# Kernel tuning notes

Hardware: AMD Instinct MI355X
Metric: run time of the kernel (lower is better)

Reference implementation:

```python
import jax, jax.numpy as jnp
import numpy as np

# Model dims (ViT-Base @ 384)
L, H, D, HD, M, P, IMG, B, NC, CH = 12, 12, 768, 64, 3072, 16, 384, 32, 1000, 3
NPATCH = (IMG // P) ** 2  # 576
SCALE = 1.0 / np.sqrt(HD)


def setup_inputs() -> dict:
    key = jax.random.key(0)
    ks = iter(jax.random.split(key, 16))
    def n(shape, s=0.02):
        return (jax.random.normal(next(ks), shape, jnp.float32) * s).astype(jnp.float32)
    return dict(
        x=jax.random.normal(next(ks), (B, CH, IMG, IMG), jnp.float32),
        conv_w=n((D, CH, P, P)), conv_b=jnp.zeros((D,), jnp.float32),
        cls_token=jnp.zeros((1, 1, D), jnp.float32),
        pos_emb=n((1, NPATCH + 1, D), 1.0),
        ln1_g=jnp.ones((L, D), jnp.float32), ln1_b=jnp.zeros((L, D), jnp.float32),
        wqkv=n((L, H, D, 3 * HD)), bqkv=jnp.zeros((L, H, 3 * HD), jnp.float32),
        wmsa=n((L, D, D)), bmsa=jnp.zeros((L, D), jnp.float32),
        ln2_g=jnp.ones((L, D), jnp.float32), ln2_b=jnp.zeros((L, D), jnp.float32),
        lnm_g=jnp.ones((L, D), jnp.float32), lnm_b=jnp.zeros((L, D), jnp.float32),
        w1=n((L, D, M)), b1=jnp.zeros((L, M), jnp.float32),
        w2=n((L, M, D)), b2=jnp.zeros((L, D), jnp.float32),
        lnf_g=jnp.ones((D,), jnp.float32), lnf_b=jnp.zeros((D,), jnp.float32),
        whead=n((D, NC)), bhead=jnp.zeros((NC,), jnp.float32),
    )


def _ln(x, g, b, eps=1e-5):
    mu = jnp.mean(x, axis=-1, keepdims=True)
    var = jnp.mean(jnp.square(x - mu), axis=-1, keepdims=True)
    return (x - mu) * jax.lax.rsqrt(var + eps) * g + b


def _encoder_block(x, p):
    (ln1_g, ln1_b, wqkv, bqkv, wmsa, bmsa,
     ln2_g, ln2_b, lnm_g, lnm_b, w1, b1, w2, b2) = p
    b = x.shape[0]
    h = _ln(x, ln1_g, ln1_b)
    # batched per-head QKV (math identical to looping over H small Linears)
    qkv = jnp.einsum('bsd,hde->bhse', h, wqkv) + bqkv[:, None, :]  # [B,H,S,3*HD]
    q, k, v = jnp.split(qkv, 3, axis=-1)
    attn = jax.nn.softmax(jnp.einsum('bhqe,bhke->bhqk', q, k) * SCALE, axis=-1)
    o = jnp.einsum('bhqk,bhke->bhqe', attn, v)          # [B,H,S,HD]
    o = o.transpose(0, 2, 1, 3).reshape(b, -1, D)        # concat heads along feature
    msa = jnp.einsum('bsd,de->bse', o, wmsa) + bmsa
    x1 = h + msa                                          # residual around MSA (post-LN1)
    h2 = _ln(x1, ln2_g, ln2_b)
    h2 = _ln(h2, lnm_g, lnm_b)                            # MLPBlock's own LayerNorm (double LN, faithful)
    mlp = jnp.einsum('bsm,md->bsd', jax.nn.gelu(jnp.einsum('bsd,dm->bsm', h2, w1) + b1, approximate=False), w2) + b2
    return x1 + mlp, None


def reference(x, conv_w, conv_b, cls_token, pos_emb,
              ln1_g, ln1_b, wqkv, bqkv, wmsa, bmsa,
              ln2_g, ln2_b, lnm_g, lnm_b, w1, b1, w2, b2,
              lnf_g, lnf_b, whead, bhead):
    b = x.shape[0]
    # patchify conv (image divisible by patch, so F.pad is a no-op)
    t = jax.lax.conv_general_dilated(x, conv_w, (P, P), 'VALID',
                                     dimension_numbers=('NCHW', 'OIHW', 'NCHW'))
    t = t + conv_b[None, :, None, None]
    # faithful to torch .view(b, -1, embed_dim) on NCHW layout (channel-major flatten)
    t = t.reshape(b, -1, D)
    n = t.shape[1]
    t = jnp.concatenate([jnp.broadcast_to(cls_token, (b, 1, D)), t], axis=1)
    t = t + pos_emb[:, :n + 1]
    stacked = (ln1_g, ln1_b, wqkv, bqkv, wmsa, bmsa,
               ln2_g, ln2_b, lnm_g, lnm_b, w1, b1, w2, b2)
    t, _ = jax.lax.scan(_encoder_block, t, stacked)
    y = _ln(t[:, 0], lnf_g, lnf_b)
    y = jax.nn.softmax(jnp.einsum('bd,dc->bc', y, whead) + bhead, axis=-1)
    return y
```

## Files before the change

kernel.cpp:

```cpp
#include <hip/hip_runtime.h>

using f16   = _Float16;
using f16x8 = __attribute__((ext_vector_type(8))) _Float16;
using f32x4 = __attribute__((ext_vector_type(4))) float;

#define MPAD  18560
#define MREAL 18464
#define MCONV 18432
#define SEQ   577
#define SPAD  640
#define NHEAD 12
#define NBATCH 32
#define SCALE_ 0.125f

__device__ __forceinline__ void load_lds16(const void* g, void* l) {
  __builtin_amdgcn_global_load_lds(
      (const __attribute__((address_space(1))) void*)g,
      (__attribute__((address_space(3))) void*)l, 16, 0, 0);
}

template<int K, int EPI>
__global__ __launch_bounds__(256) void gemm_k(
    const f16* __restrict__ A, const f16* __restrict__ Bt,
    const float* __restrict__ bias, const float* __restrict__ res,
    float* __restrict__ o32, f16* __restrict__ o16a, f16* __restrict__ o16b,
    f16* __restrict__ o16c, const float* __restrict__ pos, int N, int Mreal)
{
  static_assert(K % 64 == 0, "BK=64");
  __shared__ __align__(16) f16 As[128 * 64];
  __shared__ __align__(16) f16 Bs[128 * 64];
  const int tid = threadIdx.x;
  const int lane = tid & 63, wv = tid >> 6;

  const int gx = gridDim.x, gy = gridDim.y;
  const int nwg = gx * gy;
  const int flat = blockIdx.y * gx + blockIdx.x;
  const int xcd = flat & 7;
  const int qq = nwg >> 3, rr = nwg & 7;
  const int pos_ = ((xcd < rr) ? xcd * (qq + 1) : rr * (qq + 1) + (xcd - rr) * qq)
                   + (flat >> 3);
  const int bxi = pos_ / gy, byi = pos_ - bxi * gy;
  const int bm = byi << 7, bn = bxi << 7;

  const int wm = (wv >> 1) << 6, wn = (wv & 1) << 6;
  const int r16 = lane & 15, g4 = lane >> 4;
  const f32x4 Z4 = {0.f, 0.f, 0.f, 0.f};

  f32x4 acc[4][4];
#pragma unroll
  for (int m = 0; m < 4; ++m)
#pragma unroll
    for (int n = 0; n < 4; ++n) acc[m][n] = Z4;

  const int srow = lane >> 3;
  const int sgc  = (lane & 7) ^ srow;

  for (int k0 = 0; k0 < K; k0 += 64) {
#pragma unroll
    for (int j = 0; j < 4; ++j) {
      int rb = (wv * 4 + j) * 8;
      load_lds16(A  + (size_t)(bm + rb + srow) * K + k0 + sgc * 8, As + (wv * 4 + j) * 512);
      load_lds16(Bt + (size_t)(bn + rb + srow) * K + k0 + sgc * 8, Bs + (wv * 4 + j) * 512);
    }
    __syncthreads();
#pragma unroll
    for (int ks = 0; ks < 2; ++ks) {
      f16x8 af[4], bf[4];
#pragma unroll
      for (int m = 0; m < 4; ++m) {
        int row = wm + m * 16 + r16;
        af[m] = *(const f16x8*)(As + row * 64 + ((((ks << 2) | g4) ^ (row & 7)) << 3));
      }
#pragma unroll
      for (int n = 0; n < 4; ++n) {
        int row = wn + n * 16 + r16;
        bf[n] = *(const f16x8*)(Bs + row * 64 + ((((ks << 2) | g4) ^ (row & 7)) << 3));
      }
#pragma unroll
      for (int m = 0; m < 4; ++m)
#pragma unroll
        for (int n = 0; n < 4; ++n)
          acc[m][n] = __builtin_amdgcn_mfma_f32_16x16x32_f16(af[m], bf[n], acc[m][n], 0, 0, 0);
    }
    __syncthreads();
  }

#pragma unroll
  for (int m = 0; m < 4; ++m) {
#pragma unroll
    for (int n = 0; n < 4; ++n) {
#pragma unroll
      for (int r = 0; r < 4; ++r) {
        int grow = bm + wm + m * 16 + g4 * 4 + r;
        int gcol = bn + wn + n * 16 + r16;
        float v = acc[m][n][r];
        if constexpr (EPI == 0) {
          if (grow < Mreal) {
            int b = grow / 576, p = grow - b * 576;
            int i = gcol * 576 + p;
            int sp = i / 768, dd = i - sp * 768;
            o32[((size_t)(b * SEQ + sp + 1)) * 768 + dd] =
                v + bias[gcol] + pos[(size_t)(sp + 1) * 768 + dd];
          }
        } else if constexpr (EPI == 1) {
          if (grow < Mreal) {
            int b = grow / SEQ, s = grow - b * SEQ;
            int hq = gcol / 192, rem = gcol - hq * 192;
            int sel = rem >> 6, e = rem & 63;
            float val = v + bias[gcol];
            int bh = b * NHEAD + hq;
            if (sel == 0)      o16a[((size_t)bh * SPAD + s) * 64 + e] = (f16)val;
            else if (sel == 1) o16b[((size_t)bh * SPAD + s) * 64 + e] = (f16)val;
            else               o16c[((size_t)bh * 64 + e) * SPAD + s] = (f16)val;
          }
        } else if constexpr (EPI == 2) {
          size_t idx = (size_t)grow * N + gcol;
          o32[idx] = v + bias[gcol] + res[idx];
        } else {
          float val = v + bias[gcol];
          float gl = 0.5f * val * (1.0f + erff(val * 0.70710678f));
          o16a[(size_t)grow * N + gcol] = (f16)gl;
        }
      }
    }
  }
}

__device__ __forceinline__ void block_red2(float& a, float& b, float* sm, int tid) {
  __syncthreads();
#pragma unroll
  for (int d = 32; d; d >>= 1) { a += __shfl_down(a, d); b += __shfl_down(b, d); }
  if ((tid & 63) == 0) { int w = tid >> 6; sm[w] = a; sm[w + 4] = b; }
  __syncthreads();
  a = sm[0] + sm[1] + sm[2] + sm[3];
  b = sm[4] + sm[5] + sm[6] + sm[7];
}

__global__ __launch_bounds__(256) void ln_fwd(const float* __restrict__ X,
    const float* __restrict__ g, const float* __restrict__ bb,
    float* __restrict__ ho, f16* __restrict__ hh)
{
  int row = blockIdx.x, tid = threadIdx.x;
  const float* x = X + (size_t)row * 768;
  float v0 = x[tid], v1 = x[tid + 256], v2 = x[tid + 512];
  float s = v0 + v1 + v2, s2 = v0*v0 + v1*v1 + v2*v2;
  __shared__ float sm[8];
  block_red2(s, s2, sm, tid);
  float mu = s * (1.f/768.f);
  float var = s2 * (1.f/768.f) - mu * mu;
  float rs = rsqrtf(var + 1e-5f);
  size_t base = (size_t)row * 768;
  float y0 = (v0 - mu) * rs * g[tid      ] + bb[tid      ];
  float y1 = (v1 - mu) * rs * g[tid + 256] + bb[tid + 256];
  float y2 = (v2 - mu) * rs * g[tid + 512] + bb[tid + 512];
  ho[base + tid] = y0; ho[base + tid + 256] = y1; ho[base + tid + 512] = y2;
  hh[base + tid] = (f16)y0; hh[base + tid + 256] = (f16)y1; hh[base + tid + 512] = (f16)y2;
}

__global__ __launch_bounds__(256) void ln2_fwd(const float* __restrict__ X,
    const float* __restrict__ g2, const float* __restrict__ bb2,
    const float* __restrict__ gm, const float* __restrict__ bbm,
    f16* __restrict__ hh)
{
  int row = blockIdx.x, tid = threadIdx.x;
  const float* x = X + (size_t)row * 768;
  float v0 = x[tid], v1 = x[tid + 256], v2 = x[tid + 512];
  float s = v0 + v1 + v2, s2 = v0*v0 + v1*v1 + v2*v2;
  __shared__ float sm[8];
  block_red2(s, s2, sm, tid);
  float mu = s * (1.f/768.f), var = s2 * (1.f/768.f) - mu * mu;
  float rs = rsqrtf(var + 1e-5f);
  float y0 = (v0 - mu) * rs * g2[tid      ] + bb2[tid      ];
  float y1 = (v1 - mu) * rs * g2[tid + 256] + bb2[tid + 256];
  float y2 = (v2 - mu) * rs * g2[tid + 512] + bb2[tid + 512];
  s = y0 + y1 + y2; s2 = y0*y0 + y1*y1 + y2*y2;
  block_red2(s, s2, sm, tid);
  mu = s * (1.f/768.f); var = s2 * (1.f/768.f) - mu * mu;
  rs = rsqrtf(var + 1e-5f);
  size_t base = (size_t)row * 768;
  hh[base + tid      ] = (f16)((y0 - mu) * rs * gm[tid      ] + bbm[tid      ]);
  hh[base + tid + 256] = (f16)((y1 - mu) * rs * gm[tid + 256] + bbm[tid + 256]);
  hh[base + tid + 512] = (f16)((y2 - mu) * rs * gm[tid + 512] + bbm[tid + 512]);
}

__global__ __launch_bounds__(256) void attn_k(const f16* __restrict__ qbuf,
    const f16* __restrict__ kbuf, const f16* __restrict__ vtbuf,
    f16* __restrict__ obuf)
{
  const int bh = blockIdx.y;
  const int b = bh / NHEAD, hd = bh - b * NHEAD;
  const int s0 = blockIdx.x << 6;
  const int tid = threadIdx.x, lane = tid & 63, wv = tid >> 6;
  const int r16 = lane & 15, g4 = lane >> 4;
  const f16* Q  = qbuf  + (size_t)bh * SPAD * 64;
  const f16* Kg = kbuf  + (size_t)bh * SPAD * 64;
  const f16* Vg = vtbuf + (size_t)bh * 64 * SPAD;
  __shared__ __align__(16) f16 Kt[64 * 64];
  __shared__ __align__(16) f16 Vt[64 * 64];
  __shared__ __align__(16) f16 Pw[4][16][72];
  const f32x4 Z4 = {0.f, 0.f, 0.f, 0.f};

  f16x8 qf[2];
  {
    const f16* qr = Q + (size_t)(s0 + wv * 16 + r16) * 64;
    qf[0] = *(const f16x8*)(qr + g4 * 8);
    qf[1] = *(const f16x8*)(qr + 32 + g4 * 8);
  }
  float m_run[4] = {-1e30f, -1e30f, -1e30f, -1e30f};
  float l_run[4] = {0.f, 0.f, 0.f, 0.f};
  f32x4 o_acc[4];
#pragma unroll
  for (int n = 0; n < 4; ++n) o_acc[n] = Z4;

  for (int kt = 0; kt < SPAD; kt += 64) {
#pragma unroll
    for (int j = 0; j < 2; ++j) {
      int off = (wv * 2 + j) * 1024 + lane * 16;
      int row = off >> 7;
      int cs  = (off >> 4) & 7;
      int gc  = cs ^ (row & 7);
      load_lds16(Kg + (size_t)(kt + row) * 64 + gc * 8, (void*)((char*)Kt + (wv*2 + j) * 1024));
      load_lds16(Vg + (size_t)row * SPAD + kt + gc * 8, (void*)((char*)Vt + (wv*2 + j) * 1024));
    }
    __syncthreads();

    f32x4 sa[4];
#pragma unroll
    for (int n = 0; n < 4; ++n) sa[n] = Z4;
#pragma unroll
    for (int n = 0; n < 4; ++n) {
      int krow = n * 16 + r16;
#pragma unroll
      for (int kc = 0; kc < 2; ++kc) {
        f16x8 kf = *(const f16x8*)(Kt + krow * 64 + (((kc * 4 + g4) ^ (krow & 7)) << 3));
        sa[n] = __builtin_amdgcn_mfma_f32_16x16x32_f16(qf[kc], kf, sa[n], 0, 0, 0);
      }
    }
#pragma unroll
    for (int r = 0; r < 4; ++r) {
      float mx = -1e30f;
#pragma unroll
      for (int n = 0; n < 4; ++n) {
        int key = kt + n * 16 + r16;
        float sv = (key < SEQ) ? sa[n][r] * SCALE_ : -1e30f;
        sa[n][r] = sv;
        mx = fmaxf(mx, sv);
      }
#pragma unroll
      for (int d = 1; d < 16; d <<= 1) mx = fmaxf(mx, __shfl_xor(mx, d));
      float mnew = fmaxf(m_run[r], mx);
      float alpha = __expf(m_run[r] - mnew);
      m_run[r] = mnew;
      float ssum = 0.f;
#pragma unroll
      for (int n = 0; n < 4; ++n) {
        float p = __expf(sa[n][r] - mnew);
        ssum += p;
        Pw[wv][g4 * 4 + r][n * 16 + r16] = (f16)p;
      }
#pragma unroll
      for (int d = 1; d < 16; d <<= 1) ssum += __shfl_xor(ssum, d);
      l_run[r] = l_run[r] * alpha + ssum;
#pragma unroll
      for (int n = 0; n < 4; ++n) o_acc[n][r] *= alpha;
    }
    f16x8 pf[2];
    pf[0] = *(const f16x8*)(&Pw[wv][r16][g4 * 8]);
    pf[1] = *(const f16x8*)(&Pw[wv][r16][32 + g4 * 8]);
#pragma unroll
    for (int n = 0; n < 4; ++n) {
      int erow = n * 16 + r16;
#pragma unroll
      for (int kc = 0; kc < 2; ++kc) {
        f16x8 vf = *(const f16x8*)(Vt + erow * 64 + (((kc * 4 + g4) ^ (erow & 7)) << 3));
        o_acc[n] = __builtin_amdgcn_mfma_f32_16x16x32_f16(pf[kc], vf, o_acc[n], 0, 0, 0);
      }
    }
    __syncthreads();
  }
  float inv[4];
#pragma unroll
  for (int r = 0; r < 4; ++r) inv[r] = 1.f / l_run[r];
#pragma unroll
  for (int n = 0; n < 4; ++n)
#pragma unroll
    for (int r = 0; r < 4; ++r) {
      int s = s0 + wv * 16 + g4 * 4 + r;
      if (s < SEQ)
        obuf[((size_t)(b * SEQ + s)) * 768 + hd * 64 + n * 16 + r16] =
            (f16)(o_acc[n][r] * inv[r]);
    }
}

__global__ __launch_bounds__(256) void cvt_transpose(const float* __restrict__ in,
    f16* __restrict__ out, int K, int N, size_t ls_in, size_t ls_out)
{
  in  += (size_t)blockIdx.z * ls_in;
  out += (size_t)blockIdx.z * ls_out;
  __shared__ float t[32][33];
  int n0 = blockIdx.x << 5, k0 = blockIdx.y << 5;
  int tx = threadIdx.x & 31, ty = threadIdx.x >> 5;
#pragma unroll
  for (int i = 0; i < 4; ++i) t[ty + 8*i][tx] = in[(size_t)(k0 + ty + 8*i) * N + n0 + tx];
  __syncthreads();
#pragma unroll
  for (int i = 0; i < 4; ++i) out[(size_t)(n0 + ty + 8*i) * K + k0 + tx] = (f16)t[tx][ty + 8*i];
}

__global__ __launch_bounds__(256) void cvt_qkvw(const float* __restrict__ in,
    f16* __restrict__ out, size_t ls_in, size_t ls_out)
{
  in  += (size_t)blockIdx.z * ls_in;
  out += (size_t)blockIdx.z * ls_out;
  __shared__ float t[32][33];
  int n0 = blockIdx.x << 5, k0 = blockIdx.y << 5;
  int tx = threadIdx.x & 31, ty = threadIdx.x >> 5;
  int hq = n0 / 192, r0 = n0 - hq * 192;
#pragma unroll
  for (int i = 0; i < 4; ++i)
    t[ty + 8*i][tx] = in[(size_t)hq * 147456 + (size_t)(k0 + ty + 8*i) * 192 + r0 + tx];
  __syncthreads();
#pragma unroll
  for (int i = 0; i < 4; ++i) out[(size_t)(n0 + ty + 8*i) * 768 + k0 + tx] = (f16)t[tx][ty + 8*i];
}

__global__ __launch_bounds__(256) void cvt_plain(const float* __restrict__ in,
    f16* __restrict__ out, int n)
{
  int i = blockIdx.x * 1024 + threadIdx.x;
#pragma unroll
  for (int j = 0; j < 4; ++j) { int idx = i + j * 256; if (idx < n) out[idx] = (f16)in[idx]; }
}

__global__ __launch_bounds__(256) void zero_vpad(f16* __restrict__ vtb) {
  int bh = blockIdx.x;
  for (int idx = threadIdx.x; idx < 64 * (SPAD - SEQ); idx += 256) {
    int e = idx / (SPAD - SEQ), s = SEQ + idx - e * (SPAD - SEQ);
    vtb[((size_t)bh * 64 + e) * SPAD + s] = (f16)0.f;
  }
}

__global__ __launch_bounds__(256) void im2col_k(const float* __restrict__ x, f16* __restrict__ out) {
  int row = blockIdx.x;
  int b = row / 576, p = row - b * 576;
  int py = p / 24, px = p - py * 24;
  int tid = threadIdx.x;
#pragma unroll
  for (int j = 0; j < 3; ++j) {
    int k = tid + j * 256;
    int c = k >> 8, rem = k & 255;
    int iy = rem >> 4, ix = rem & 15;
    out[(size_t)row * 768 + k] =
        (f16)x[(((size_t)(b * 3 + c)) * 384 + py * 16 + iy) * 384 + px * 16 + ix];
  }
}

__global__ __launch_bounds__(256) void cls_k(const float* __restrict__ ct,
    const float* __restrict__ pos, float* __restrict__ X)
{
  int b = blockIdx.x, tid = threadIdx.x;
#pragma unroll
  for (int j = 0; j < 3; ++j) {
    int d0 = tid + j * 256;
    X[((size_t)b * SEQ) * 768 + d0] = ct[d0] + pos[d0];
  }
}

__global__ __launch_bounds__(256) void head_k(const float* __restrict__ X,
    const float* __restrict__ g, const float* __restrict__ bb,
    const float* __restrict__ W, const float* __restrict__ bhd,
    float* __restrict__ out)
{
  int b = blockIdx.x, tid = threadIdx.x;
  const float* x = X + (size_t)(b * SEQ) * 768;
  float v0 = x[tid], v1 = x[tid + 256], v2 = x[tid + 512];
  float s = v0 + v1 + v2, s2 = v0*v0 + v1*v1 + v2*v2;
  __shared__ float sm[8];
  block_red2(s, s2, sm, tid);
  float mu = s * (1.f/768.f), var = s2 * (1.f/768.f) - mu * mu;
  float rs = rsqrtf(var + 1e-5f);
  __shared__ float y[768];
  y[tid      ] = (v0 - mu) * rs * g[tid      ] + bb[tid      ];
  y[tid + 256] = (v1 - mu) * rs * g[tid + 256] + bb[tid + 256];
  y[tid + 512] = (v2 - mu) * rs * g[tid + 512] + bb[tid + 512];
  __syncthreads();
  float lg[4];
#pragma unroll
  for (int j = 0; j < 4; ++j) {
    int c = tid + j * 256;
    float acc = (c < 1000) ? bhd[c] : -1e30f;
    if (c < 1000)
      for (int d = 0; d < 768; ++d) acc = fmaf(y[d], W[(size_t)d * 1000 + c], acc);
    lg[j] = acc;
  }
  float mx = fmaxf(fmaxf(lg[0], lg[1]), fmaxf(lg[2], lg[3]));
#pragma unroll
  for (int d = 32; d; d >>= 1) mx = fmaxf(mx, __shfl_down(mx, d));
  if ((tid & 63) == 0) sm[tid >> 6] = mx;
  __syncthreads();
  mx = fmaxf(fmaxf(sm[0], sm[1]), fmaxf(sm[2], sm[3]));
  float ex[4], se = 0.f;
#pragma unroll
  for (int j = 0; j < 4; ++j) {
    int c = tid + j * 256;
    ex[j] = (c < 1000) ? __expf(lg[j] - mx) : 0.f;
    se += ex[j];
  }
  __syncthreads();
#pragma unroll
  for (int d = 32; d; d >>= 1) se += __shfl_down(se, d);
  if ((tid & 63) == 0) sm[tid >> 6] = se;
  __syncthreads();
  se = sm[0] + sm[1] + sm[2] + sm[3];
  float inv = 1.f / se;
#pragma unroll
  for (int j = 0; j < 4; ++j) {
    int c = tid + j * 256;
    if (c < 1000) out[(size_t)b * 1000 + c] = ex[j] * inv;
  }
}

extern "C" void kernel_launch(void* const* d_in, const int* in_sizes, int n_in,
                              void* d_out, int out_size, void* d_ws, size_t ws_size,
                              hipStream_t stream)
{
  (void)in_sizes; (void)n_in; (void)out_size;
  const float* x      = (const float*)d_in[0];
  const float* conv_w = (const float*)d_in[1];
  const float* conv_b = (const float*)d_in[2];
  const float* cls_t  = (const float*)d_in[3];
  const float* pos    = (const float*)d_in[4];
  const float* ln1_g  = (const float*)d_in[5];
  const float* ln1_b  = (const float*)d_in[6];
  const float* wqkv   = (const float*)d_in[7];
  const float* bqkv   = (const float*)d_in[8];
  const float* wmsa   = (const float*)d_in[9];
  const float* bmsa   = (const float*)d_in[10];
  const float* ln2_g  = (const float*)d_in[11];
  const float* ln2_b  = (const float*)d_in[12];
  const float* lnm_g  = (const float*)d_in[13];
  const float* lnm_b  = (const float*)d_in[14];
  const float* w1     = (const float*)d_in[15];
  const float* b1     = (const float*)d_in[16];
  const float* w2     = (const float*)d_in[17];
  const float* b2     = (const float*)d_in[18];
  const float* lnf_g  = (const float*)d_in[19];
  const float* lnf_b  = (const float*)d_in[20];
  const float* whead  = (const float*)d_in[21];
  const float* bhead  = (const float*)d_in[22];
  float* out = (float*)d_out;

  const size_t szQ  = (size_t)2304 * 768;
  const size_t szM  = (size_t)768 * 768;
  const size_t szW1 = (size_t)3072 * 768;
  const size_t szW2 = (size_t)768 * 3072;
  const size_t fixed_bytes =
      (size_t)MPAD * 768 * 4 + (size_t)MPAD * 768 * 4 + (size_t)MPAD * 768 * 2 +
      (size_t)MPAD * 3072 * 2 + 3 * ((size_t)NBATCH * NHEAD * SPAD * 64 * 2) +
      (size_t)768 * 768 * 2  + 16 * 256 ;
  const bool hoist =
      ws_size >= fixed_bytes + 12 * (szQ + szM + szW1 + szW2) * 2 + 8 * 256;
  const int LW = hoist ? 12 : 1;

  char* wsp = (char*)d_ws;
  size_t off = 0;
  auto alloc = [&](size_t bytes) {
    char* p = wsp + off; off += (bytes + 255) & ~(size_t)255; return p;
  };
  float* X    = (float*)alloc((size_t)MPAD * 768 * 4);
  float* hbf  = (float*)alloc((size_t)MPAD * 768 * 4);
  f16*   hh   = (f16*)  alloc((size_t)MPAD * 768 * 2);
  f16*   abuf = (f16*)  alloc((size_t)MPAD * 3072 * 2);
  f16*   qb   = (f16*)  alloc((size_t)NBATCH * NHEAD * SPAD * 64 * 2);
  f16*   kb   = (f16*)  alloc((size_t)NBATCH * NHEAD * SPAD * 64 * 2);
  f16*   vtb  = (f16*)  alloc((size_t)NBATCH * NHEAD * SPAD * 64 * 2);
  f16*   WcT  = (f16*)  alloc((size_t)768 * 768 * 2);
  f16*   WqkvT= (f16*)  alloc(LW * szQ  * 2);
  f16*   WmsaT= (f16*)  alloc(LW * szM  * 2);
  f16*   W1T  = (f16*)  alloc(LW * szW1 * 2);
  f16*   W2T  = (f16*)  alloc(LW * szW2 * 2);
  f16*   obuf   = abuf;
  f16*   patchA = abuf;
  f16*   h2h    = hh;
  if (ws_size < off) return;

  zero_vpad<<<dim3(NBATCH * NHEAD), 256, 0, stream>>>(vtb);
  cvt_plain<<<dim3((768 * 768 + 1023) / 1024), 256, 0, stream>>>(conv_w, WcT, 768 * 768);
  if (hoist) {
    cvt_qkvw<<<dim3(72, 24, 12), 256, 0, stream>>>(wqkv, WqkvT, (size_t)12*768*192, szQ);
    cvt_transpose<<<dim3(24, 24, 12), 256, 0, stream>>>(wmsa, WmsaT, 768, 768, szM, szM);
    cvt_transpose<<<dim3(96, 24, 12), 256, 0, stream>>>(w1, W1T, 768, 3072, szW1, szW1);
    cvt_transpose<<<dim3(24, 96, 12), 256, 0, stream>>>(w2, W2T, 3072, 768, szW2, szW2);
  }
  im2col_k<<<dim3(MCONV), 256, 0, stream>>>(x, patchA);
  gemm_k<768, 0><<<dim3(6, 144), 256, 0, stream>>>(
      patchA, WcT, conv_b, nullptr, X, nullptr, nullptr, nullptr, pos, 768, MCONV);
  cls_k<<<dim3(NBATCH), 256, 0, stream>>>(cls_t, pos, X);

  for (int l = 0; l < 12; ++l) {
    f16* wq  = WqkvT + (hoist ? (size_t)l * szQ  : 0);
    f16* wms = WmsaT + (hoist ? (size_t)l * szM  : 0);
    f16* w1t = W1T   + (hoist ? (size_t)l * szW1 : 0);
    f16* w2t = W2T   + (hoist ? (size_t)l * szW2 : 0);
    if (!hoist) {
      cvt_qkvw<<<dim3(72, 24), 256, 0, stream>>>(
          wqkv + (size_t)l * 12 * 768 * 192, wq, 0, 0);
      cvt_transpose<<<dim3(24, 24), 256, 0, stream>>>(
          wmsa + (size_t)l * 768 * 768, wms, 768, 768, 0, 0);
      cvt_transpose<<<dim3(96, 24), 256, 0, stream>>>(
          w1 + (size_t)l * 768 * 3072, w1t, 768, 3072, 0, 0);
      cvt_transpose<<<dim3(24, 96), 256, 0, stream>>>(
          w2 + (size_t)l * 3072 * 768, w2t, 3072, 768, 0, 0);
    }

    ln_fwd<<<dim3(MREAL), 256, 0, stream>>>(X, ln1_g + l * 768, ln1_b + l * 768, hbf, hh);
    gemm_k<768, 1><<<dim3(18, 145), 256, 0, stream>>>(
        hh, wq, bqkv + (size_t)l * 2304, nullptr, nullptr, qb, kb, vtb, nullptr, 2304, MREAL);
    attn_k<<<dim3(10, NBATCH * NHEAD), 256, 0, stream>>>(qb, kb, vtb, obuf);
    gemm_k<768, 2><<<dim3(6, 145), 256, 0, stream>>>(
        obuf, wms, bmsa + l * 768, hbf, X, nullptr, nullptr, nullptr, nullptr, 768, MREAL);
    ln2_fwd<<<dim3(MREAL), 256, 0, stream>>>(
        X, ln2_g + l * 768, ln2_b + l * 768, lnm_g + l * 768, lnm_b + l * 768, h2h);
    gemm_k<768, 3><<<dim3(24, 145), 256, 0, stream>>>(
        h2h, w1t, b1 + (size_t)l * 3072, nullptr, nullptr, abuf, nullptr, nullptr, nullptr, 3072, MREAL);
    gemm_k<3072, 2><<<dim3(6, 145), 256, 0, stream>>>(
        abuf, w2t, b2 + l * 768, X, X, nullptr, nullptr, nullptr, nullptr, 768, MREAL);
  }
  head_k<<<dim3(NBATCH), 256, 0, stream>>>(X, lnf_g, lnf_b, whead, bhead, out);
}
```

Baseline: 9.352 ms.

## Rewrite GEMM as 256x256 tiles with double-buffered LDS prefetch and 512 threads

The GEMM kernel moves from 128x128 tiles with 256 threads and a single LDS buffer to 256x256 tiles with 512 threads (8 waves) and double-buffered LDS. Global-to-LDS loads for the next K-step are interleaved between MFMA groups, using explicit vmcnt waits, barriers and setprio. The aim is to hide memory latency and get more reuse per tile. In exchange the grid is smaller (fewer workgroups for 256 CUs), LDS use is higher at 128KB per block, the accumulators need more registers, and activation buffers are padded to a larger MPAD.

New measurement: 9.177 ms. About the same (-1.9%).

```diff
diff --git a/kernel.cpp b/kernel.cpp
--- a/kernel.cpp
+++ b/kernel.cpp
@@ -4,7 +4,7 @@
 using f16x8 = __attribute__((ext_vector_type(8))) _Float16;
 using f32x4 = __attribute__((ext_vector_type(4))) float;
 
-#define MPAD  18560
+#define MPAD2 18688
 #define MREAL 18464
 #define MCONV 18432
 #define SEQ   577
@@ -20,99 +20,156 @@
 }
 
 template<int K, int EPI>
-__global__ __launch_bounds__(256) void gemm_k(
+__global__ __launch_bounds__(512, 2) void gemm_k(
     const f16* __restrict__ A, const f16* __restrict__ Bt,
     const float* __restrict__ bias, const float* __restrict__ res,
     float* __restrict__ o32, f16* __restrict__ o16a, f16* __restrict__ o16b,
     f16* __restrict__ o16c, const float* __restrict__ pos, int N, int Mreal)
 {
   static_assert(K % 64 == 0, "BK=64");
-  __shared__ __align__(16) f16 As[128 * 64];
-  __shared__ __align__(16) f16 Bs[128 * 64];
+  constexpr int NT = K / 64;
+  __shared__ __align__(16) f16 As[2][256 * 64];
+  __shared__ __align__(16) f16 Bs[2][256 * 64];
   const int tid = threadIdx.x;
   const int lane = tid & 63, wv = tid >> 6;
 
-  const int gx = gridDim.x, gy = gridDim.y;
-  const int nwg = gx * gy;
+  const int gx = gridDim.x;
+  const int nwg = gx * gridDim.y;
   const int flat = blockIdx.y * gx + blockIdx.x;
   const int xcd = flat & 7;
   const int qq = nwg >> 3, rr = nwg & 7;
-  const int pos_ = ((xcd < rr) ? xcd * (qq + 1) : rr * (qq + 1) + (xcd - rr) * qq)
-                   + (flat >> 3);
-  const int bxi = pos_ / gy, byi = pos_ - bxi * gy;
-  const int bm = byi << 7, bn = bxi << 7;
-
-  const int wm = (wv >> 1) << 6, wn = (wv & 1) << 6;
+  const int p_ = ((xcd < rr) ? xcd * (qq + 1) : rr * (qq + 1) + (xcd - rr) * qq)
+                 + (flat >> 3);
+  const int byi = p_ / gx, bxi = p_ - byi * gx;
+  const int bm = byi << 8, bn = bxi << 8;
+
+  const int wm = (wv >> 2) << 7;
+  const int wn = (wv & 3) << 6;
   const int r16 = lane & 15, g4 = lane >> 4;
   const f32x4 Z4 = {0.f, 0.f, 0.f, 0.f};
 
-  f32x4 acc[4][4];
-#pragma unroll
-  for (int m = 0; m < 4; ++m)
+  f32x4 acc[8][4];
+#pragma unroll
+  for (int m = 0; m < 8; ++m)
 #pragma unroll
     for (int n = 0; n < 4; ++n) acc[m][n] = Z4;
 
-  const int srow = lane >> 3;
-  const int sgc  = (lane & 7) ^ srow;
-
-  for (int k0 = 0; k0 < K; k0 += 64) {
-#pragma unroll
-    for (int j = 0; j < 4; ++j) {
-      int rb = (wv * 4 + j) * 8;
-      load_lds16(A  + (size_t)(bm + rb + srow) * K + k0 + sgc * 8, As + (wv * 4 + j) * 512);
-      load_lds16(Bt + (size_t)(bn + rb + srow) * K + k0 + sgc * 8, Bs + (wv * 4 + j) * 512);
-    }
-    __syncthreads();
-#pragma unroll
-    for (int ks = 0; ks < 2; ++ks) {
-      f16x8 af[4], bf[4];
-#pragma unroll
-      for (int m = 0; m < 4; ++m) {
-        int row = wm + m * 16 + r16;
-        af[m] = *(const f16x8*)(As + row * 64 + ((((ks << 2) | g4) ^ (row & 7)) << 3));
-      }
-#pragma unroll
-      for (int n = 0; n < 4; ++n) {
-        int row = wn + n * 16 + r16;
-        bf[n] = *(const f16x8*)(Bs + row * 64 + ((((ks << 2) | g4) ^ (row & 7)) << 3));
-      }
-#pragma unroll
-      for (int m = 0; m < 4; ++m)
-#pragma unroll
-        for (int n = 0; n < 4; ++n)
-          acc[m][n] = __builtin_amdgcn_mfma_f32_16x16x32_f16(af[m], bf[n], acc[m][n], 0, 0, 0);
-    }
-    __syncthreads();
-  }
-
-#pragma unroll
-  for (int m = 0; m < 4; ++m) {
-#pragma unroll
-    for (int n = 0; n < 4; ++n) {
+  const int srow = tid >> 3;
+  const int sgc  = (tid & 7) ^ (srow & 7);
+  const f16* Ag = A  + (size_t)(bm + srow) * K + sgc * 8;
+  const f16* Bg = Bt + (size_t)(bn + srow) * K + sgc * 8;
+  const int ldso = wv << 9;
+
+  auto stA = [&](int buf, int r0, int k0) {
+    load_lds16(Ag + (size_t)r0 * K + k0, &As[buf][r0 * 64 + ldso]);
+  };
+  auto stB = [&](int buf, int r0, int k0) {
+    load_lds16(Bg + (size_t)r0 * K + k0, &Bs[buf][r0 * 64 + ldso]);
+  };
+  auto rdfrag = [&](const f16* base, int row, f16x8& lo, f16x8& hi) {
+    const f16* p = base + row * 64;
+    lo = *(const f16x8*)(p + ((g4 ^ (row & 7)) << 3));
+    hi = *(const f16x8*)(p + (((4 | g4) ^ (row & 7)) << 3));
+  };
+
+  stB(0, 0, 0); stB(0, 64, 0); stB(0, 128, 0); stB(0, 192, 0);
+  stA(0, 0, 0); stA(0, 128, 0);
+  stA(0, 64, 0); stA(0, 192, 0);
+  asm volatile("s_waitcnt vmcnt(2)" ::: "memory");
+  __builtin_amdgcn_s_barrier();
+
+#pragma unroll 1
+  for (int t = 0; t < NT; ++t) {
+    const f16* Ac = As[t & 1];
+    const f16* Bc = Bs[t & 1];
+    const int nb = (t + 1) & 1;
+    const int k0n = (t + 1) << 6;
+    const bool pf = (t + 1 < NT);
+
+    f16x8 bf[4][2];
+#pragma unroll
+    for (int nt = 0; nt < 4; ++nt) rdfrag(Bc, wn + nt * 16 + r16, bf[nt][0], bf[nt][1]);
+
+    f16x8 a0l, a0h, a1l, a1h;
+    rdfrag(Ac, wm + 0 * 16 + r16, a0l, a0h);
+    rdfrag(Ac, wm + 1 * 16 + r16, a1l, a1h);
+    if (pf) { stB(nb, 0, k0n); stB(nb, 64, k0n); }
+    __builtin_amdgcn_s_setprio(1);
+#pragma unroll
+    for (int nt = 0; nt < 4; ++nt) {
+      acc[0][nt] = __builtin_amdgcn_mfma_f32_16x16x32_f16(a0l, bf[nt][0], acc[0][nt], 0, 0, 0);
+      acc[0][nt] = __builtin_amdgcn_mfma_f32_16x16x32_f16(a0h, bf[nt][1], acc[0][nt], 0, 0, 0);
+      acc[1][nt] = __builtin_amdgcn_mfma_f32_16x16x32_f16(a1l, bf[nt][0], acc[1][nt], 0, 0, 0);
+      acc[1][nt] = __builtin_amdgcn_mfma_f32_16x16x32_f16(a1h, bf[nt][1], acc[1][nt], 0, 0, 0);
+    }
+    __builtin_amdgcn_s_setprio(0);
+    rdfrag(Ac, wm + 2 * 16 + r16, a0l, a0h);
+    rdfrag(Ac, wm + 3 * 16 + r16, a1l, a1h);
+    if (pf) { stB(nb, 128, k0n); stB(nb, 192, k0n); }
+    __builtin_amdgcn_s_setprio(1);
+#pragma unroll
+    for (int nt = 0; nt < 4; ++nt) {
+      acc[2][nt] = __builtin_amdgcn_mfma_f32_16x16x32_f16(a0l, bf[nt][0], acc[2][nt], 0, 0, 0);
+      acc[2][nt] = __builtin_amdgcn_mfma_f32_16x16x32_f16(a0h, bf[nt][1], acc[2][nt], 0, 0, 0);
+      acc[3][nt] = __builtin_amdgcn_mfma_f32_16x16x32_f16(a1l, bf[nt][0], acc[3][nt], 0, 0, 0);
+      acc[3][nt] = __builtin_amdgcn_mfma_f32_16x16x32_f16(a1h, bf[nt][1], acc[3][nt], 0, 0, 0);
+    }
+    __builtin_amdgcn_s_setprio(0);
+    asm volatile("s_waitcnt vmcnt(4)" ::: "memory");
+    __builtin_amdgcn_s_barrier();
+    rdfrag(Ac, wm + 4 * 16 + r16, a0l, a0h);
+    rdfrag(Ac, wm + 5 * 16 + r16, a1l, a1h);
+    if (pf) { stA(nb, 0, k0n); stA(nb, 128, k0n); }
+    __builtin_amdgcn_s_setprio(1);
+#pragma unroll
+    for (int nt = 0; nt < 4; ++nt) {
+      acc[4][nt] = __builtin_amdgcn_mfma_f32_16x16x32_f16(a0l, bf[nt][0], acc[4][nt], 0, 0, 0);
+      acc[4][nt] = __builtin_amdgcn_mfma_f32_16x16x32_f16(a0h, bf[nt][1], acc[4][nt], 0, 0, 0);
+      acc[5][nt] = __builtin_amdgcn_mfma_f32_16x16x32_f16(a1l, bf[nt][0], acc[5][nt], 0, 0, 0);
+      acc[5][nt] = __builtin_amdgcn_mfma_f32_16x16x32_f16(a1h, bf[nt][1], acc[5][nt], 0, 0, 0);
+    }
+    __builtin_amdgcn_s_setprio(0);
+    rdfrag(Ac, wm + 6 * 16 + r16, a0l, a0h);
+    rdfrag(Ac, wm + 7 * 16 + r16, a1l, a1h);
+    if (pf) { stA(nb, 64, k0n); stA(nb, 192, k0n); }
+    __builtin_amdgcn_s_setprio(1);
+#pragma unroll
+    for (int nt = 0; nt < 4; ++nt) {
+      acc[6][nt] = __builtin_amdgcn_mfma_f32_16x16x32_f16(a0l, bf[nt][0], acc[6][nt], 0, 0, 0);
+      acc[6][nt] = __builtin_amdgcn_mfma_f32_16x16x32_f16(a0h, bf[nt][1], acc[6][nt], 0, 0, 0);
+      acc[7][nt] = __builtin_amdgcn_mfma_f32_16x16x32_f16(a1l, bf[nt][0], acc[7][nt], 0, 0, 0);
+      acc[7][nt] = __builtin_amdgcn_mfma_f32_16x16x32_f16(a1h, bf[nt][1], acc[7][nt], 0, 0, 0);
+    }
+    __builtin_amdgcn_s_setprio(0);
+    asm volatile("s_waitcnt vmcnt(2)" ::: "memory");
+    __builtin_amdgcn_s_barrier();
+  }
+
+#pragma unroll
+  for (int mt = 0; mt < 8; ++mt) {
+#pragma unroll
+    for (int nt = 0; nt < 4; ++nt) {
 #pragma unroll
       for (int r = 0; r < 4; ++r) {
-        int grow = bm + wm + m * 16 + g4 * 4 + r;
-        int gcol = bn + wn + n * 16 + r16;
-        float v = acc[m][n][r];
+        int grow = bm + wm + mt * 16 + g4 * 4 + r;
+        int gcol = bn + wn + nt * 16 + r16;
+        if (grow >= Mreal) continue;
+        float v = acc[mt][nt][r];
         if constexpr (EPI == 0) {
-          if (grow < Mreal) {
-            int b = grow / 576, p = grow - b * 576;
-            int i = gcol * 576 + p;
-            int sp = i / 768, dd = i - sp * 768;
-            o32[((size_t)(b * SEQ + sp + 1)) * 768 + dd] =
-                v + bias[gcol] + pos[(size_t)(sp + 1) * 768 + dd];
-          }
+          int b = grow / 576, p = grow - b * 576;
+          int i = gcol * 576 + p;
+          int sp = i / 768, dd = i - sp * 768;
+          o32[((size_t)(b * SEQ + sp + 1)) * 768 + dd] =
+              v + bias[gcol] + pos[(size_t)(sp + 1) * 768 + dd];
         } else if constexpr (EPI == 1) {
-          if (grow < Mreal) {
-            int b = grow / SEQ, s = grow - b * SEQ;
-            int hq = gcol / 192, rem = gcol - hq * 192;
-            int sel = rem >> 6, e = rem & 63;
-            float val = v + bias[gcol];
-            int bh = b * NHEAD + hq;
-            if (sel == 0)      o16a[((size_t)bh * SPAD + s) * 64 + e] = (f16)val;
-            else if (sel == 1) o16b[((size_t)bh * SPAD + s) * 64 + e] = (f16)val;
-            else               o16c[((size_t)bh * 64 + e) * SPAD + s] = (f16)val;
-          }
+          int b = grow / SEQ, s = grow - b * SEQ;
+          int hq = gcol / 192, rem = gcol - hq * 192;
+          int sel = rem >> 6, e = rem & 63;
+          float val = v + bias[gcol];
+          int bh = b * NHEAD + hq;
+          if (sel == 0)      o16a[((size_t)bh * SPAD + s) * 64 + e] = (f16)val;
+          else if (sel == 1) o16b[((size_t)bh * SPAD + s) * 64 + e] = (f16)val;
+          else               o16c[((size_t)bh * 64 + e) * SPAD + s] = (f16)val;
         } else if constexpr (EPI == 2) {
           size_t idx = (size_t)grow * N + gcol;
           o32[idx] = v + bias[gcol] + res[idx];
@@ -455,8 +512,8 @@
   const size_t szW1 = (size_t)3072 * 768;
   const size_t szW2 = (size_t)768 * 3072;
   const size_t fixed_bytes =
-      (size_t)MPAD * 768 * 4 + (size_t)MPAD * 768 * 4 + (size_t)MPAD * 768 * 2 +
-      (size_t)MPAD * 3072 * 2 + 3 * ((size_t)NBATCH * NHEAD * SPAD * 64 * 2) +
+      (size_t)MPAD2 * 768 * 4 + (size_t)MPAD2 * 768 * 4 + (size_t)MPAD2 * 768 * 2 +
+      (size_t)MPAD2 * 3072 * 2 + 3 * ((size_t)NBATCH * NHEAD * SPAD * 64 * 2) +
       (size_t)768 * 768 * 2  + 16 * 256 ;
   const bool hoist =
       ws_size >= fixed_bytes + 12 * (szQ + szM + szW1 + szW2) * 2 + 8 * 256;
@@ -467,10 +524,10 @@
   auto alloc = [&](size_t bytes) {
     char* p = wsp + off; off += (bytes + 255) & ~(size_t)255; return p;
   };
-  float* X    = (float*)alloc((size_t)MPAD * 768 * 4);
-  float* hbf  = (float*)alloc((size_t)MPAD * 768 * 4);
-  f16*   hh   = (f16*)  alloc((size_t)MPAD * 768 * 2);
-  f16*   abuf = (f16*)  alloc((size_t)MPAD * 3072 * 2);
+  float* X    = (float*)alloc((size_t)MPAD2 * 768 * 4);
+  float* hbf  = (float*)alloc((size_t)MPAD2 * 768 * 4);
+  f16*   hh   = (f16*)  alloc((size_t)MPAD2 * 768 * 2);
+  f16*   abuf = (f16*)  alloc((size_t)MPAD2 * 3072 * 2);
   f16*   qb   = (f16*)  alloc((size_t)NBATCH * NHEAD * SPAD * 64 * 2);
   f16*   kb   = (f16*)  alloc((size_t)NBATCH * NHEAD * SPAD * 64 * 2);
   f16*   vtb  = (f16*)  alloc((size_t)NBATCH * NHEAD * SPAD * 64 * 2);
@@ -493,7 +550,7 @@
     cvt_transpose<<<dim3(24, 96, 12), 256, 0, stream>>>(w2, W2T, 3072, 768, szW2, szW2);
   }
   im2col_k<<<dim3(MCONV), 256, 0, stream>>>(x, patchA);
-  gemm_k<768, 0><<<dim3(6, 144), 256, 0, stream>>>(
+  gemm_k<768, 0><<<dim3(3, 72), 512, 0, stream>>>(
       patchA, WcT, conv_b, nullptr, X, nullptr, nullptr, nullptr, pos, 768, MCONV);
   cls_k<<<dim3(NBATCH), 256, 0, stream>>>(cls_t, pos, X);
 
@@ -514,16 +571,16 @@
     }
 
     ln_fwd<<<dim3(MREAL), 256, 0, stream>>>(X, ln1_g + l * 768, ln1_b + l * 768, hbf, hh);
-    gemm_k<768, 1><<<dim3(18, 145), 256, 0, stream>>>(
+    gemm_k<768, 1><<<dim3(9, 73), 512, 0, stream>>>(
         hh, wq, bqkv + (size_t)l * 2304, nullptr, nullptr, qb, kb, vtb, nullptr, 2304, MREAL);
     attn_k<<<dim3(10, NBATCH * NHEAD), 256, 0, stream>>>(qb, kb, vtb, obuf);
-    gemm_k<768, 2><<<dim3(6, 145), 256, 0, stream>>>(
+    gemm_k<768, 2><<<dim3(3, 73), 512, 0, stream>>>(
         obuf, wms, bmsa + l * 768, hbf, X, nullptr, nullptr, nullptr, nullptr, 768, MREAL);
     ln2_fwd<<<dim3(MREAL), 256, 0, stream>>>(
         X, ln2_g + l * 768, ln2_b + l * 768, lnm_g + l * 768, lnm_b + l * 768, h2h);
-    gemm_k<768, 3><<<dim3(24, 145), 256, 0, stream>>>(
+    gemm_k<768, 3><<<dim3(12, 73), 512, 0, stream>>>(
         h2h, w1t, b1 + (size_t)l * 3072, nullptr, nullptr, abuf, nullptr, nullptr, nullptr, 3072, MREAL);
-    gemm_k<3072, 2><<<dim3(6, 145), 256, 0, stream>>>(
+    gemm_k<3072, 2><<<dim3(3, 73), 512, 0, stream>>>(
         abuf, w2t, b2 + l * 768, X, X, nullptr, nullptr, nullptr, nullptr, 768, MREAL);
   }
   head_k<<<dim3(NBATCH), 256, 0, stream>>>(X, lnf_g, lnf_b, whead, bhead, out);
```

## Halve GEMM K-tile to 32 and raster workgroups in column bands of six

Applied to the files above, without the earlier changes.

The GEMM kernel now stages 32-wide K slices instead of 64, with a matching 4-way XOR swizzle for the LDS layout. This halves shared memory per block, which could allow more resident workgroups. The tile-index mapping now walks column bands six tiles wide so concurrently running blocks share B tiles in L2. The cost is twice as many barriers and global load rounds per K, and less MFMA work between each sync.

Result: faster. 8.300 ms (-11.2%).

```diff
diff --git a/kernel.cpp b/kernel.cpp
--- a/kernel.cpp
+++ b/kernel.cpp
@@ -26,9 +26,8 @@
     float* __restrict__ o32, f16* __restrict__ o16a, f16* __restrict__ o16b,
     f16* __restrict__ o16c, const float* __restrict__ pos, int N, int Mreal)
 {
-  static_assert(K % 64 == 0, "BK=64");
-  __shared__ __align__(16) f16 As[128 * 64];
-  __shared__ __align__(16) f16 Bs[128 * 64];
+  __shared__ __align__(16) f16 As[128*32];
+  __shared__ __align__(16) f16 Bs[128*32];
   const int tid = threadIdx.x;
   const int lane = tid & 63, wv = tid >> 6;
 
@@ -37,9 +36,12 @@
   const int flat = blockIdx.y * gx + blockIdx.x;
   const int xcd = flat & 7;
   const int qq = nwg >> 3, rr = nwg & 7;
-  const int pos_ = ((xcd < rr) ? xcd * (qq + 1) : rr * (qq + 1) + (xcd - rr) * qq)
-                   + (flat >> 3);
-  const int bxi = pos_ / gy, byi = pos_ - bxi * gy;
+  const int p_ = ((xcd < rr) ? xcd * (qq + 1) : rr * (qq + 1) + (xcd - rr) * qq)
+                 + (flat >> 3);
+  const int bandsz = gy * 6;
+  const int band = p_ / bandsz, within = p_ - band * bandsz;
+  const int byi = within / 6;
+  const int bxi = band * 6 + (within - byi * 6);
   const int bm = byi << 7, bn = bxi << 7;
 
   const int wm = (wv >> 1) << 6, wn = (wv & 1) << 6;
@@ -52,36 +54,34 @@
 #pragma unroll
     for (int n = 0; n < 4; ++n) acc[m][n] = Z4;
 
-  const int srow = lane >> 3;
-  const int sgc  = (lane & 7) ^ srow;
-
-  for (int k0 = 0; k0 < K; k0 += 64) {
-#pragma unroll
-    for (int j = 0; j < 4; ++j) {
-      int rb = (wv * 4 + j) * 8;
-      load_lds16(A  + (size_t)(bm + rb + srow) * K + k0 + sgc * 8, As + (wv * 4 + j) * 512);
-      load_lds16(Bt + (size_t)(bn + rb + srow) * K + k0 + sgc * 8, Bs + (wv * 4 + j) * 512);
+  const int soff = wv * 1024 + lane * 8;
+  for (int k0 = 0; k0 < K; k0 += 32) {
+#pragma unroll
+    for (int j = 0; j < 2; ++j) {
+      int off = soff + j * 512;
+      int row = off >> 5;
+      int cs  = (off >> 3) & 3;
+      int gc  = cs ^ (row & 3);
+      load_lds16(A  + (size_t)(bm + row) * K + k0 + gc * 8, As + (wv*2 + j) * 512);
+      load_lds16(Bt + (size_t)(bn + row) * K + k0 + gc * 8, Bs + (wv*2 + j) * 512);
     }
     __syncthreads();
-#pragma unroll
-    for (int ks = 0; ks < 2; ++ks) {
-      f16x8 af[4], bf[4];
-#pragma unroll
-      for (int m = 0; m < 4; ++m) {
-        int row = wm + m * 16 + r16;
-        af[m] = *(const f16x8*)(As + row * 64 + ((((ks << 2) | g4) ^ (row & 7)) << 3));
-      }
-#pragma unroll
-      for (int n = 0; n < 4; ++n) {
-        int row = wn + n * 16 + r16;
-        bf[n] = *(const f16x8*)(Bs + row * 64 + ((((ks << 2) | g4) ^ (row & 7)) << 3));
-      }
-#pragma unroll
-      for (int m = 0; m < 4; ++m)
-#pragma unroll
-        for (int n = 0; n < 4; ++n)
-          acc[m][n] = __builtin_amdgcn_mfma_f32_16x16x32_f16(af[m], bf[n], acc[m][n], 0, 0, 0);
-    }
+    f16x8 af[4], bf[4];
+#pragma unroll
+    for (int m = 0; m < 4; ++m) {
+      int row = wm + m * 16 + r16;
+      af[m] = *(const f16x8*)(As + row * 32 + ((g4 ^ (row & 3)) << 3));
+    }
+#pragma unroll
+    for (int n = 0; n < 4; ++n) {
+      int row = wn + n * 16 + r16;
+      bf[n] = *(const f16x8*)(Bs + row * 32 + ((g4 ^ (row & 3)) << 3));
+    }
+#pragma unroll
+    for (int m = 0; m < 4; ++m)
+#pragma unroll
+      for (int n = 0; n < 4; ++n)
+        acc[m][n] = __builtin_amdgcn_mfma_f32_16x16x32_f16(af[m], bf[n], acc[m][n], 0, 0, 0);
     __syncthreads();
   }
 
```
